# Performance work log

Hardware: AMD Instinct MI355X
Metric: run time of the kernel (lower is better)

## Reference

```python
import jax, jax.numpy as jnp
import numpy as np

LN_EPS = 1e-5
N_HEADS = 8

def _layernorm(x, g, b):
    mu = jnp.mean(x, axis=-1, keepdims=True)
    var = jnp.var(x, axis=-1, keepdims=True)
    return (x - mu) * jax.lax.rsqrt(var + LN_EPS) * g + b

def _posenc(seqlen, d_model, dtype):
    den = jnp.exp(-jnp.arange(0, d_model, 2, dtype=dtype) * (np.log(10000.0) / d_model))
    pos = jnp.arange(seqlen, dtype=dtype)[:, None]  # [S,1]
    pe = jnp.zeros((seqlen, d_model), dtype=dtype)
    pe = pe.at[:, 0::2].set(jnp.sin(pos * den))
    pe = pe.at[:, 1::2].set(jnp.cos(pos * den)[:, : d_model // 2])
    return pe  # [S,d]

def setup_inputs() -> dict:
    key = jax.random.key(0)
    ks = jax.random.split(key, 12)
    B, S, V, D, F, L, DL = 64, 256, 16, 512, 2048, 6, 256
    s = 0.05
    return {
        "src_pad": jax.random.normal(ks[0], (B, S, V), jnp.float32),
        "emb_w": jax.random.normal(ks[1], (D, V), jnp.float32) * s,
        "emb_b": jnp.zeros((D,), jnp.float32),
        "qkv_w": jax.random.normal(ks[2], (L, 3 * D, D), jnp.float32) * s,
        "qkv_b": jnp.zeros((L, 3 * D), jnp.float32),
        "out_w": jax.random.normal(ks[3], (L, D, D), jnp.float32) * s,
        "out_b": jnp.zeros((L, D), jnp.float32),
        "ff1_w": jax.random.normal(ks[4], (L, F, D), jnp.float32) * s,
        "ff1_b": jnp.zeros((L, F), jnp.float32),
        "ff2_w": jax.random.normal(ks[5], (L, D, F), jnp.float32) * s,
        "ff2_b": jnp.zeros((L, D), jnp.float32),
        "ln1_g": jnp.ones((L, D), jnp.float32),
        "ln1_b": jnp.zeros((L, D), jnp.float32),
        "ln2_g": jnp.ones((L, D), jnp.float32),
        "ln2_b": jnp.zeros((L, D), jnp.float32),
        "lat_w": jax.random.normal(ks[6], (DL, S * D), jnp.float32) * 0.005,
        "lat_b": jnp.zeros((DL,), jnp.float32),
        "head_w": jax.random.normal(ks[7], (1, DL), jnp.float32) * s,
        "head_b": jnp.zeros((1,), jnp.float32),
    }

def reference(src_pad, emb_w, emb_b, qkv_w, qkv_b, out_w, out_b,
              ff1_w, ff1_b, ff2_w, ff2_b, ln1_g, ln1_b, ln2_g, ln2_b,
              lat_w, lat_b, head_w, head_b):
    B, S, V = src_pad.shape
    D = emb_w.shape[0]
    L = qkv_w.shape[0]
    H = N_HEADS
    dh = D // H
    # batched replacement of the per-token Python-loop embedding
    x = jnp.einsum('bsv,dv->bsd', src_pad, emb_w) + emb_b
    x = x + _posenc(S, D, x.dtype)  # dropout is identity at eval
    scale = 1.0 / np.sqrt(dh)
    for l in range(L):  # post-norm PyTorch TransformerEncoderLayer, relu FFN
        qkv = jnp.einsum('bsd,ed->bse', x, qkv_w[l]) + qkv_b[l]  # [B,S,3D]
        q, k, v = jnp.split(qkv, 3, axis=-1)
        q = q.reshape(B, S, H, dh).transpose(0, 2, 1, 3)
        k = k.reshape(B, S, H, dh).transpose(0, 2, 1, 3)
        v = v.reshape(B, S, H, dh).transpose(0, 2, 1, 3)
        attn = jax.nn.softmax(jnp.einsum('bhqd,bhkd->bhqk', q, k) * scale, axis=-1)
        o = jnp.einsum('bhqk,bhkd->bhqd', attn, v).transpose(0, 2, 1, 3).reshape(B, S, D)
        o = jnp.einsum('bsd,ed->bse', o, out_w[l]) + out_b[l]
        x = _layernorm(x + o, ln1_g[l], ln1_b[l])
        h = jax.nn.relu(jnp.einsum('bsd,fd->bsf', x, ff1_w[l]) + ff1_b[l])
        h = jnp.einsum('bsf,df->bsd', h, ff2_w[l]) + ff2_b[l]
        x = _layernorm(x + h, ln2_g[l], ln2_b[l])
    mem = x.reshape(B, S * D) @ lat_w.T + lat_b  # [B, d_latent]
    pred = jax.nn.sigmoid(mem @ head_w.T + head_b)  # [B,1]
    return pred
```

## Files before the change

### kernel.cpp

```cpp
#include <hip/hip_runtime.h>
#include <hip/hip_bf16.h>
#include <cstdint>

#define DEV static __device__ __forceinline__

typedef __attribute__((ext_vector_type(8))) short bf16x8;
typedef __attribute__((ext_vector_type(4))) float f32x4;

DEV unsigned short f2bf(float f) {
  union { float f; unsigned u; } c; c.f = f;
  unsigned u = c.u;
  return (unsigned short)((u + 0x7fffu + ((u >> 16) & 1u)) >> 16);
}
DEV float bf2f(unsigned short h) {
  union { unsigned u; float f; } c; c.u = ((unsigned)h) << 16; return c.f;
}
DEV float bflo(unsigned u) { union { unsigned u; float f; } c; c.u = u << 16; return c.f; }
DEV float bfhi(unsigned u) { union { unsigned u; float f; } c; c.u = u & 0xffff0000u; return c.f; }
DEV unsigned pack_bf16(float a, float b) {
  union { float f; unsigned u; } ca, cb; ca.f = a; cb.f = b;
  return __builtin_amdgcn_perm(cb.u + 0x8000u, ca.u + 0x8000u, 0x07060302u);
}

#define ASYNC_COPY16(gsrc, ldst)                                                      \
  __builtin_amdgcn_global_load_lds(                                                   \
      (const __attribute__((address_space(1))) void*)(unsigned long long)(gsrc),      \
      (__attribute__((address_space(3))) void*)(unsigned int)(unsigned long long)(ldst), \
      16, 0, 0)

__global__ void cvt_all_kernel(const float* __restrict__ s0, unsigned short* __restrict__ d0,
                               const float* __restrict__ s1, unsigned short* __restrict__ d1,
                               const float* __restrict__ s2, unsigned short* __restrict__ d2,
                               const float* __restrict__ s3, unsigned short* __restrict__ d3) {
  const int blk = blockIdx.x;
  const float* s; unsigned short* d; int base;
  if (blk < 4608)       { s = s0; d = d0; base = blk; }
  else if (blk < 6144)  { s = s1; d = d1; base = blk - 4608; }
  else if (blk < 12288) { s = s2; d = d2; base = blk - 6144; }
  else                  { s = s3; d = d3; base = blk - 12288; }
  size_t i = ((size_t)base * 256 + threadIdx.x) * 4;
  float4 v = *(const float4*)(s + i);
  d[i + 0] = f2bf(v.x);
  d[i + 1] = f2bf(v.y);
  d[i + 2] = f2bf(v.z);
  d[i + 3] = f2bf(v.w);
}

__global__ void embed_kernel(const float* __restrict__ src,
                             const float* __restrict__ emb_w,
                             const float* __restrict__ emb_b,
                             unsigned short* __restrict__ xb) {
  const int bs = blockIdx.x;
  const int d = threadIdx.x;
  const int s = bs & 255;
  __shared__ float sv[16];
  if (d < 16) sv[d] = src[(size_t)bs * 16 + d];
  __syncthreads();
  const float* wr = emb_w + (size_t)d * 16;
  float acc = emb_b[d];
#pragma unroll
  for (int v = 0; v < 16; v++) acc += sv[v] * wr[v];
  const float den = __expf(-(float)(d & ~1) * (9.2103403719761836f / 512.f));
  const float arg = (float)s * den;
  acc += (d & 1) ? __cosf(arg) : __sinf(arg);
  xb[(size_t)bs * 512 + d] = f2bf(acc);
}

template <int RELU>
__global__ __launch_bounds__(256, 3) void gemm_nt(
    const unsigned short* __restrict__ A,
    const unsigned short* __restrict__ B,
    const float* __restrict__ bias,
    unsigned short* __restrict__ Cb,
    int M, int N, int K) {
  constexpr int MT = 4;
  constexpr int NT = 4;
  __shared__ unsigned short As[128 * 64];
  __shared__ unsigned short Bs[128 * 64];
  const int tid = threadIdx.x;
  const int lane = tid & 63;
  const int w = tid >> 6;
  const int m0 = blockIdx.x * 128;
  const int n0 = blockIdx.y * 128;

  const int srow = lane >> 3;
  const int scol = (((lane & 7) ^ srow)) * 8;
  const unsigned short* gA0 = A + (size_t)(m0 + w * 32 + srow) * K + scol;
  unsigned short* lA0 = As + (w * 32) * 64;
  const unsigned short* gB0 = B + (size_t)(n0 + w * 32 + srow) * K + scol;
  unsigned short* lB0 = Bs + (w * 32) * 64;

  const int wm = (w >> 1) * 64;
  const int wn = (w & 1) * 64;
  const int r16 = lane & 15;
  const int quad = lane >> 4;
  const int rsw = r16 & 7;

  f32x4 acc[MT][NT] = {};

  for (int k0 = 0; k0 < K; k0 += 64) {
#pragma unroll
    for (int i = 0; i < 4; i++)
      ASYNC_COPY16(gA0 + (size_t)(i * 8) * K + k0, lA0 + i * 512);
#pragma unroll
    for (int i = 0; i < 4; i++)
      ASYNC_COPY16(gB0 + (size_t)(i * 8) * K + k0, lB0 + i * 512);
    asm volatile("s_waitcnt vmcnt(0)" ::: "memory");
    __syncthreads();
#pragma unroll
    for (int kh = 0; kh < 2; kh++) {
      const int ko = ((kh * 4 + quad) ^ rsw) * 8;
      bf16x8 xa[MT], wb[NT];
#pragma unroll
      for (int i = 0; i < MT; i++)
        xa[i] = *(const bf16x8*)(As + (wm + i * 16 + r16) * 64 + ko);
#pragma unroll
      for (int j = 0; j < NT; j++)
        wb[j] = *(const bf16x8*)(Bs + (wn + j * 16 + r16) * 64 + ko);
#pragma unroll
      for (int i = 0; i < MT; i++)
#pragma unroll
        for (int j = 0; j < NT; j++)
          acc[i][j] = __builtin_amdgcn_mfma_f32_16x16x32_bf16(wb[j], xa[i], acc[i][j], 0, 0, 0);
    }
    __syncthreads();
  }

  const int mb = m0 + wm + r16;
  const int nb = n0 + wn + quad * 4;
#pragma unroll
  for (int j = 0; j < NT; j++) {
    const int n = nb + j * 16;
    const float4 bv = *(const float4*)(bias + n);
#pragma unroll
    for (int i = 0; i < MT; i++) {
      const size_t off = (size_t)(mb + i * 16) * N + n;
      float4 v;
      v.x = acc[i][j][0] + bv.x;
      v.y = acc[i][j][1] + bv.y;
      v.z = acc[i][j][2] + bv.z;
      v.w = acc[i][j][3] + bv.w;
      if (RELU) {
        v.x = fmaxf(v.x, 0.f); v.y = fmaxf(v.y, 0.f);
        v.z = fmaxf(v.z, 0.f); v.w = fmaxf(v.w, 0.f);
      }
      uint2 u;
      u.x = pack_bf16(v.x, v.y);
      u.y = pack_bf16(v.z, v.w);
      *(uint2*)(Cb + off) = u;
    }
  }
}

__global__ __launch_bounds__(512, 2) void gemm_ln(
    const unsigned short* __restrict__ A,
    const unsigned short* __restrict__ B,
    const float* __restrict__ bias,
    const float* __restrict__ g,
    const float* __restrict__ beta,
    unsigned short* __restrict__ xb,
    int K) {
  constexpr int BM = 64;
  constexpr int MT = 4;
  constexpr int NT = 4;
  constexpr int NL = 1 + 8;
  constexpr int BUFE = (BM + 512) * 64;
  __shared__ unsigned short lds[2 * BUFE];

  const int tid = threadIdx.x;
  const int lane = tid & 63;
  const int w = tid >> 6;
  const int r16 = lane & 15;
  const int quad = lane >> 4;
  const int rsw = r16 & 7;
  const int m0 = blockIdx.x * BM;

  const int srow = tid >> 3;
  const int scol = ((tid & 7) ^ (srow & 7)) * 8;
  const unsigned short* gA = A + (size_t)(m0 + srow) * K + scol;
  const unsigned short* gB = B + (size_t)srow * K + scol;

#define STG2(i, bufi, kc)                                                       \
  do {                                                                          \
    if ((i) == 0)                                                               \
      ASYNC_COPY16(gA + (size_t)(kc), lds + (bufi) * BUFE + (w * 8) * 64);      \
    else                                                                        \
      ASYNC_COPY16(gB + (size_t)(((i) - 1) * 64) * K + (kc),                    \
                   lds + (bufi) * BUFE + (BM + ((i) - 1) * 64 + w * 8) * 64);   \
  } while (0)

  f32x4 acc[MT][NT] = {};

  const int NK = K >> 6;
#pragma unroll
  for (int i = 0; i < NL; ++i) STG2(i, 0, 0);

  for (int kt = 0; kt < NK; ++kt) {
    const int buf = kt & 1;
    if (kt + 1 < NK) {
      const int kc = (kt + 1) << 6;
#pragma unroll
      for (int i = 0; i < NL; ++i) STG2(i, buf ^ 1, kc);
      asm volatile("s_waitcnt vmcnt(%0)" ::"i"(NL) : "memory");
    } else {
      asm volatile("s_waitcnt vmcnt(0)" ::: "memory");
    }
    __builtin_amdgcn_s_barrier();
    const unsigned short* As = lds + buf * BUFE;
    const unsigned short* Bs = As + BM * 64;
#pragma unroll
    for (int kh = 0; kh < 2; ++kh) {
      const int ko = ((kh * 4 + quad) ^ rsw) * 8;
      bf16x8 aR[MT], bR[NT];
#pragma unroll
      for (int m = 0; m < MT; ++m)
        aR[m] = *(const bf16x8*)(As + (m * 16 + r16) * 64 + ko);
#pragma unroll
      for (int j = 0; j < NT; ++j)
        bR[j] = *(const bf16x8*)(Bs + (w * 64 + j * 16 + r16) * 64 + ko);
      __builtin_amdgcn_s_setprio(1);
#pragma unroll
      for (int m = 0; m < MT; ++m)
#pragma unroll
        for (int j = 0; j < NT; ++j)
          acc[m][j] = __builtin_amdgcn_mfma_f32_16x16x32_bf16(
              bR[j], aR[m], acc[m][j], 0, 0, 0);
      __builtin_amdgcn_s_setprio(0);
    }
    asm volatile("s_waitcnt lgkmcnt(0)" ::: "memory");
    __builtin_amdgcn_s_barrier();
  }
#undef STG2

  const int nb = w * 64 + quad * 4;
  float psum[MT] = {}, psq[MT] = {};
#pragma unroll
  for (int j = 0; j < NT; ++j) {
    const int n = nb + j * 16;
    const float4 bv = *(const float4*)(bias + n);
#pragma unroll
    for (int i = 0; i < MT; ++i) {
      const size_t off = (size_t)(m0 + i * 16 + r16) * 512 + n;
      const uint2 ru = *(const uint2*)(xb + off);
      f32x4 v;
      v[0] = acc[i][j][0] + bv.x + bflo(ru.x);
      v[1] = acc[i][j][1] + bv.y + bfhi(ru.x);
      v[2] = acc[i][j][2] + bv.z + bflo(ru.y);
      v[3] = acc[i][j][3] + bv.w + bfhi(ru.y);
      acc[i][j] = v;
#pragma unroll
      for (int r = 0; r < 4; ++r) {
        psum[i] += v[r];
        psq[i] += v[r] * v[r];
      }
    }
  }
#pragma unroll
  for (int i = 0; i < MT; ++i) {
    psum[i] += __shfl_xor(psum[i], 16);
    psum[i] += __shfl_xor(psum[i], 32);
    psq[i] += __shfl_xor(psq[i], 16);
    psq[i] += __shfl_xor(psq[i], 32);
  }
  float* redS = (float*)lds;
  float* redQ = redS + 512;
  if (quad == 0) {
#pragma unroll
    for (int i = 0; i < MT; ++i) {
      redS[w * 64 + i * 16 + r16] = psum[i];
      redQ[w * 64 + i * 16 + r16] = psq[i];
    }
  }
  __syncthreads();
  float mu[MT], rs[MT];
#pragma unroll
  for (int i = 0; i < MT; ++i) {
    const int row = i * 16 + r16;
    float s = 0.f, q = 0.f;
#pragma unroll
    for (int ww = 0; ww < 8; ++ww) {
      s += redS[ww * 64 + row];
      q += redQ[ww * 64 + row];
    }
    mu[i] = s * (1.f / 512.f);
    rs[i] = rsqrtf(q * (1.f / 512.f) - mu[i] * mu[i] + 1e-5f);
  }
#pragma unroll
  for (int j = 0; j < NT; ++j) {
    const int n = nb + j * 16;
    const float4 gv = *(const float4*)(g + n);
    const float4 be = *(const float4*)(beta + n);
#pragma unroll
    for (int i = 0; i < MT; ++i) {
      const size_t off = (size_t)(m0 + i * 16 + r16) * 512 + n;
      const f32x4 v = acc[i][j];
      float o0 = (v[0] - mu[i]) * rs[i] * gv.x + be.x;
      float o1 = (v[1] - mu[i]) * rs[i] * gv.y + be.y;
      float o2 = (v[2] - mu[i]) * rs[i] * gv.z + be.z;
      float o3 = (v[3] - mu[i]) * rs[i] * gv.w + be.w;
      uint2 u;
      u.x = pack_bf16(o0, o1);
      u.y = pack_bf16(o2, o3);
      *(uint2*)(xb + off) = u;
    }
  }
}

__global__ __launch_bounds__(256, 2) void attn_fused(
    const unsigned short* __restrict__ qkv,
    unsigned short* __restrict__ O) {
  __shared__ unsigned short Vt[64 * 264];
  __shared__ unsigned short Pl[32 * 264];
  __shared__ float redM[4][32];
  __shared__ float redS[4][32];
  const int tid = threadIdx.x;
  const int lane = tid & 63;
  const int w = tid >> 6;
  const int r16 = lane & 15;
  const int quad = lane >> 4;
  const int h = blockIdx.x & 7;
  const int b = blockIdx.x >> 3;

  {
    const int kp = w * 32 + (lane & 31);
    const int dhalf = lane >> 5;
    const unsigned short* vbase =
        qkv + (size_t)(b * 256 + 2 * kp) * 1536 + 1024 + h * 64;
    unsigned* dst = (unsigned*)Vt;
#pragma unroll
    for (int t = 0; t < 4; t++) {
      const int dc = dhalf + 2 * t;
      const uint4 a = *(const uint4*)(vbase + dc * 8);
      const uint4 bb = *(const uint4*)(vbase + 1536 + dc * 8);
      const unsigned* ap = (const unsigned*)&a;
      const unsigned* bp = (const unsigned*)&bb;
#pragma unroll
      for (int i = 0; i < 4; i++) {
        const unsigned lo = ap[i], hi = bp[i];
        dst[(dc * 8 + 2 * i) * 132 + kp] = (lo & 0xffffu) | (hi << 16);
        dst[(dc * 8 + 2 * i + 1) * 132 + kp] = (lo >> 16) | (hi & 0xffff0000u);
      }
    }
  }
  __syncthreads();

  const unsigned short* krow =
      qkv + (size_t)(b * 256 + r16) * 1536 + 512 + h * 64 + quad * 8;
  const unsigned short* qrow =
      qkv + (size_t)(b * 256 + r16) * 1536 + h * 64 + quad * 8;

  for (int qt = 0; qt < 8; qt++) {
    const int q0 = qt * 32;
    f32x4 acc[4][2] = {};
    bf16x8 bQ0[2], bQ1[2];
#pragma unroll
    for (int nt = 0; nt < 2; nt++) {
      const unsigned short* qp = qrow + (size_t)(q0 + nt * 16) * 1536;
      bQ0[nt] = *(const bf16x8*)(qp);
      bQ1[nt] = *(const bf16x8*)(qp + 32);
    }
#pragma unroll
    for (int mt = 0; mt < 4; mt++) {
      const unsigned short* kp = krow + (size_t)(w * 64 + mt * 16) * 1536;
      const bf16x8 aK0 = *(const bf16x8*)(kp);
      const bf16x8 aK1 = *(const bf16x8*)(kp + 32);
#pragma unroll
      for (int nt = 0; nt < 2; nt++) {
        acc[mt][nt] = __builtin_amdgcn_mfma_f32_16x16x32_bf16(aK0, bQ0[nt], acc[mt][nt], 0, 0, 0);
        acc[mt][nt] = __builtin_amdgcn_mfma_f32_16x16x32_bf16(aK1, bQ1[nt], acc[mt][nt], 0, 0, 0);
      }
    }
    float ml[2];
#pragma unroll
    for (int nt = 0; nt < 2; nt++) {
      float m = acc[0][nt][0];
#pragma unroll
      for (int mt = 0; mt < 4; mt++)
#pragma unroll
        for (int r = 0; r < 4; r++) m = fmaxf(m, acc[mt][nt][r]);
      m = fmaxf(m, __shfl_xor(m, 16));
      m = fmaxf(m, __shfl_xor(m, 32));
      ml[nt] = m;
      float s = 0.f;
#pragma unroll
      for (int mt = 0; mt < 4; mt++)
#pragma unroll
        for (int r = 0; r < 4; r++) {
          acc[mt][nt][r] = __expf((acc[mt][nt][r] - m) * 0.125f);
          s += acc[mt][nt][r];
        }
      s += __shfl_xor(s, 16);
      s += __shfl_xor(s, 32);
      if (quad == 0) {
        redM[w][nt * 16 + r16] = m;
        redS[w][nt * 16 + r16] = s;
      }
    }
    __syncthreads();
    float scale[2];
#pragma unroll
    for (int nt = 0; nt < 2; nt++) {
      const int q = nt * 16 + r16;
      const float m0_ = redM[0][q], m1_ = redM[1][q];
      const float m2_ = redM[2][q], m3_ = redM[3][q];
      const float mg = fmaxf(fmaxf(m0_, m1_), fmaxf(m2_, m3_));
      const float sg = redS[0][q] * __expf((m0_ - mg) * 0.125f) +
                       redS[1][q] * __expf((m1_ - mg) * 0.125f) +
                       redS[2][q] * __expf((m2_ - mg) * 0.125f) +
                       redS[3][q] * __expf((m3_ - mg) * 0.125f);
      scale[nt] = __expf((ml[nt] - mg) * 0.125f) / sg;
    }
#pragma unroll
    for (int nt = 0; nt < 2; nt++) {
      unsigned short* prow = Pl + (nt * 16 + r16) * 264 + w * 64 + quad * 4;
#pragma unroll
      for (int mt = 0; mt < 4; mt++) {
        uint2 u;
        u.x = pack_bf16(acc[mt][nt][0] * scale[nt], acc[mt][nt][1] * scale[nt]);
        u.y = pack_bf16(acc[mt][nt][2] * scale[nt], acc[mt][nt][3] * scale[nt]);
        *(uint2*)(prow + mt * 16) = u;
      }
    }
    __syncthreads();
    f32x4 o[2] = {};
#pragma unroll
    for (int s = 0; s < 8; s++) {
      const bf16x8 aV = *(const bf16x8*)(Vt + (w * 16 + r16) * 264 + s * 32 + quad * 8);
#pragma unroll
      for (int nt = 0; nt < 2; nt++) {
        const bf16x8 bP = *(const bf16x8*)(Pl + (nt * 16 + r16) * 264 + s * 32 + quad * 8);
        o[nt] = __builtin_amdgcn_mfma_f32_16x16x32_bf16(aV, bP, o[nt], 0, 0, 0);
      }
    }
#pragma unroll
    for (int nt = 0; nt < 2; nt++) {
      uint2 u;
      u.x = pack_bf16(o[nt][0], o[nt][1]);
      u.y = pack_bf16(o[nt][2], o[nt][3]);
      *(uint2*)(O + (size_t)(b * 256 + q0 + nt * 16 + r16) * 512 + h * 64 +
                w * 16 + quad * 4) = u;
    }
  }
}

__global__ void zero_kernel(float* __restrict__ p) {
  p[blockIdx.x * 256 + threadIdx.x] = 0.f;
}

__global__ __launch_bounds__(256) void latent_gemm(
    const unsigned short* __restrict__ xb, const float* __restrict__ W,
    float* __restrict__ mem) {
  const int tid = threadIdx.x;
  const int lane = tid & 63;
  const int w = tid >> 6;
  const int r16 = lane & 15;
  const int quad = lane >> 4;
  const int n0 = blockIdx.x * 64 + w * 16;
  const int kc0 = blockIdx.y * 1024;

  const float* wrow = W + (size_t)(n0 + r16) * 131072 + kc0 + quad * 8;
  const unsigned short* xrow = xb + (size_t)r16 * 131072 + kc0 + quad * 8;

  f32x4 c[4] = {};
  for (int k = 0; k < 1024; k += 32) {
    const float4 wa = *(const float4*)(wrow + k);
    const float4 wb = *(const float4*)(wrow + k + 4);
    union { unsigned u[4]; bf16x8 v; } cw;
    cw.u[0] = pack_bf16(wa.x, wa.y);
    cw.u[1] = pack_bf16(wa.z, wa.w);
    cw.u[2] = pack_bf16(wb.x, wb.y);
    cw.u[3] = pack_bf16(wb.z, wb.w);
#pragma unroll
    for (int i = 0; i < 4; i++) {
      const bf16x8 aX = *(const bf16x8*)(xrow + (size_t)i * 2097152 + k);
      c[i] = __builtin_amdgcn_mfma_f32_16x16x32_bf16(aX, cw.v, c[i], 0, 0, 0);
    }
  }
#pragma unroll
  for (int i = 0; i < 4; i++)
#pragma unroll
    for (int r = 0; r < 4; r++)
      atomicAdd(&mem[(size_t)(i * 16 + quad * 4 + r) * 256 + n0 + r16], c[i][r]);
}

__global__ __launch_bounds__(256) void head_kernel(
    const float* __restrict__ mem, const float* __restrict__ lat_b,
    const float* __restrict__ head_w, const float* __restrict__ head_b,
    float* __restrict__ out) {
  const int b = blockIdx.x;
  const int tid = threadIdx.x;
  float v = (mem[(size_t)b * 256 + tid] + lat_b[tid]) * head_w[tid];
#pragma unroll
  for (int off = 32; off > 0; off >>= 1) v += __shfl_xor(v, off);
  __shared__ float red[4];
  const int w = tid >> 6, lane = tid & 63;
  if (lane == 0) red[w] = v;
  __syncthreads();
  if (tid == 0) {
    const float z = red[0] + red[1] + red[2] + red[3] + head_b[0];
    out[b] = 1.f / (1.f + __expf(-z));
  }
}

extern "C" void kernel_launch(void* const* d_in, const int* in_sizes, int n_in,
                              void* d_out, int out_size, void* d_ws, size_t ws_size,
                              hipStream_t stream) {
  (void)in_sizes; (void)n_in; (void)out_size; (void)ws_size;
  const float* src_pad = (const float*)d_in[0];
  const float* emb_w = (const float*)d_in[1];
  const float* emb_b = (const float*)d_in[2];
  const float* qkv_w = (const float*)d_in[3];
  const float* qkv_b = (const float*)d_in[4];
  const float* out_w = (const float*)d_in[5];
  const float* out_b = (const float*)d_in[6];
  const float* ff1_w = (const float*)d_in[7];
  const float* ff1_b = (const float*)d_in[8];
  const float* ff2_w = (const float*)d_in[9];
  const float* ff2_b = (const float*)d_in[10];
  const float* ln1_g = (const float*)d_in[11];
  const float* ln1_b = (const float*)d_in[12];
  const float* ln2_g = (const float*)d_in[13];
  const float* ln2_b = (const float*)d_in[14];
  const float* lat_w = (const float*)d_in[15];
  const float* lat_b = (const float*)d_in[16];
  const float* head_w = (const float*)d_in[17];
  const float* head_b = (const float*)d_in[18];
  float* out = (float*)d_out;

  char* p = (char*)d_ws;
  unsigned short* xb = (unsigned short*)p; p += (size_t)16384 * 512 * 2;
  unsigned short* qkv = (unsigned short*)p; p += (size_t)16384 * 1536 * 2;
  unsigned short* attno = (unsigned short*)p; p += (size_t)16384 * 512 * 2;
  unsigned short* h = (unsigned short*)p;     p += (size_t)16384 * 2048 * 2;
  unsigned short* wq = (unsigned short*)p;    p += (size_t)4718592 * 2;
  unsigned short* wo = (unsigned short*)p;    p += (size_t)1572864 * 2;
  unsigned short* wf1 = (unsigned short*)p;   p += (size_t)6291456 * 2;
  unsigned short* wf2 = (unsigned short*)p;   p += (size_t)6291456 * 2;
  float* mem = (float*)p;           p += (size_t)16384 * 4;

  cvt_all_kernel<<<18432, 256, 0, stream>>>(qkv_w, wq, out_w, wo, ff1_w, wf1,
                                            ff2_w, wf2);

  embed_kernel<<<16384, 512, 0, stream>>>(src_pad, emb_w, emb_b, xb);

  for (int l = 0; l < 6; l++) {
    gemm_nt<0><<<dim3(128, 12), 256, 0, stream>>>(
        xb, wq + (size_t)l * 786432, qkv_b + (size_t)l * 1536, qkv,
        16384, 1536, 512);
    attn_fused<<<512, 256, 0, stream>>>(qkv, attno);
    gemm_ln<<<256, 512, 0, stream>>>(
        attno, wo + (size_t)l * 262144, out_b + (size_t)l * 512,
        ln1_g + (size_t)l * 512, ln1_b + (size_t)l * 512, xb, 512);
    gemm_nt<1><<<dim3(128, 16), 256, 0, stream>>>(
        xb, wf1 + (size_t)l * 1048576, ff1_b + (size_t)l * 2048, h,
        16384, 2048, 512);
    gemm_ln<<<256, 512, 0, stream>>>(
        h, wf2 + (size_t)l * 1048576, ff2_b + (size_t)l * 512,
        ln2_g + (size_t)l * 512, ln2_b + (size_t)l * 512, xb, 2048);
  }

  zero_kernel<<<64, 256, 0, stream>>>(mem);
  latent_gemm<<<dim3(4, 128), 256, 0, stream>>>(xb, lat_w, mem);
  head_kernel<<<64, 256, 0, stream>>>(mem, lat_b, head_w, head_b, out);
}
```

Before: 1.477 ms.

## Single-buffer LDS in gemm_ln to raise occupancy instead of double buffering

Removes the double-buffered LDS pipeline from the fused GEMM+LayerNorm kernel. Each k-tile is now loaded synchronously, waited on and barriered before compute, and the s_setprio hints are dropped. This halves the LDS footprint so more blocks can be resident (launch bounds raised to 4 blocks/CU). In exchange, global loads no longer overlap with MFMA work inside a block, so latency hiding depends on other resident blocks.

```diff
diff --git a/kernel.cpp b/kernel.cpp
--- a/kernel.cpp
+++ b/kernel.cpp
@@ -152,7 +152,7 @@
   }
 }
 
-__global__ __launch_bounds__(512, 2) void gemm_ln(
+__global__ __launch_bounds__(512, 4) void gemm_ln(
     const unsigned short* __restrict__ A,
     const unsigned short* __restrict__ B,
     const float* __restrict__ bias,
@@ -165,7 +165,7 @@
   constexpr int NT = 4;
   constexpr int NL = 1 + 8;
   constexpr int BUFE = (BM + 512) * 64;
-  __shared__ unsigned short lds[2 * BUFE];
+  __shared__ unsigned short lds[BUFE];
 
   const int tid = threadIdx.x;
   const int lane = tid & 63;
@@ -180,34 +180,26 @@
   const unsigned short* gA = A + (size_t)(m0 + srow) * K + scol;
   const unsigned short* gB = B + (size_t)srow * K + scol;
 
-#define STG2(i, bufi, kc)                                                       \
+#define STG2(i, kc)                                                             \
   do {                                                                          \
     if ((i) == 0)                                                               \
-      ASYNC_COPY16(gA + (size_t)(kc), lds + (bufi) * BUFE + (w * 8) * 64);      \
+      ASYNC_COPY16(gA + (size_t)(kc), lds + (w * 8) * 64);                      \
     else                                                                        \
       ASYNC_COPY16(gB + (size_t)(((i) - 1) * 64) * K + (kc),                    \
-                   lds + (bufi) * BUFE + (BM + ((i) - 1) * 64 + w * 8) * 64);   \
+                   lds + (BM + ((i) - 1) * 64 + w * 8) * 64);                   \
   } while (0)
 
   f32x4 acc[MT][NT] = {};
 
   const int NK = K >> 6;
-#pragma unroll
-  for (int i = 0; i < NL; ++i) STG2(i, 0, 0);
-
   for (int kt = 0; kt < NK; ++kt) {
-    const int buf = kt & 1;
-    if (kt + 1 < NK) {
-      const int kc = (kt + 1) << 6;
-#pragma unroll
-      for (int i = 0; i < NL; ++i) STG2(i, buf ^ 1, kc);
-      asm volatile("s_waitcnt vmcnt(%0)" ::"i"(NL) : "memory");
-    } else {
-      asm volatile("s_waitcnt vmcnt(0)" ::: "memory");
-    }
-    __builtin_amdgcn_s_barrier();
-    const unsigned short* As = lds + buf * BUFE;
-    const unsigned short* Bs = As + BM * 64;
+    const int kc = kt << 6;
+#pragma unroll
+    for (int i = 0; i < NL; ++i) STG2(i, kc);
+    asm volatile("s_waitcnt vmcnt(0)" ::: "memory");
+    __syncthreads();
+    const unsigned short* As = lds;
+    const unsigned short* Bs = lds + BM * 64;
 #pragma unroll
     for (int kh = 0; kh < 2; ++kh) {
       const int ko = ((kh * 4 + quad) ^ rsw) * 8;
@@ -218,17 +210,14 @@
 #pragma unroll
       for (int j = 0; j < NT; ++j)
         bR[j] = *(const bf16x8*)(Bs + (w * 64 + j * 16 + r16) * 64 + ko);
-      __builtin_amdgcn_s_setprio(1);
 #pragma unroll
       for (int m = 0; m < MT; ++m)
 #pragma unroll
         for (int j = 0; j < NT; ++j)
           acc[m][j] = __builtin_amdgcn_mfma_f32_16x16x32_bf16(
               bR[j], aR[m], acc[m][j], 0, 0, 0);
-      __builtin_amdgcn_s_setprio(0);
-    }
-    asm volatile("s_waitcnt lgkmcnt(0)" ::: "memory");
-    __builtin_amdgcn_s_barrier();
+    }
+    __syncthreads();
   }
 #undef STG2
 
```

After: 1.506 ms. About the same (+2.0%).
